# Performance work log

Measured on AMD Instinct MI355X. Metric: run time of the kernel, lower is better.

## Reference

```python
import jax, jax.numpy as jnp
import numpy as np

EMB = 1024
NUM_HEADS = 16


def setup_inputs() -> dict:
    key = jax.random.key(0)
    k_x, k_k, k_q, k_v, k_u, k_b = jax.random.split(key, 6)
    b, s, e = 4, 2048, EMB
    lim = 1.0 / np.sqrt(e)
    return {
        "x": jax.random.normal(k_x, (b, s, e), dtype=jnp.float32),
        "Wk": jax.random.uniform(k_k, (e, e), jnp.float32, -lim, lim),
        "Wq": jax.random.uniform(k_q, (e, e), jnp.float32, -lim, lim),
        "Wv": jax.random.uniform(k_v, (e, e), jnp.float32, -lim, lim),
        "Wu": jax.random.uniform(k_u, (e, e), jnp.float32, -lim, lim),
        "bu": jax.random.uniform(k_b, (e,), jnp.float32, -lim, lim),
    }


def reference(x, Wk, Wq, Wv, Wu, bu):
    b, s, e = x.shape
    h = NUM_HEADS
    d = e // h
    # scale q and k each by emb**(-1/4), as in the original (note: emb, not head_size)
    scale = e ** -0.25
    # project and split heads: (b, h, s, d)
    q = (x @ Wq.T).reshape(b, s, h, d).transpose(0, 2, 1, 3) * scale
    k = (x @ Wk.T).reshape(b, s, h, d).transpose(0, 2, 1, 3) * scale
    v = (x @ Wv.T).reshape(b, s, h, d).transpose(0, 2, 1, 3)
    # attention scores (b, h, s, s)
    dot = jnp.einsum("bhqd,bhkd->bhqk", q, k)
    # causal mask: strictly-upper triangle (offset=1) set to -inf
    causal = jnp.triu(jnp.ones((s, s), dtype=bool), k=1)
    dot = jnp.where(causal[None, None, :, :], -jnp.inf, dot)
    attn = jax.nn.softmax(dot, axis=-1)
    out = jnp.einsum("bhqk,bhkd->bhqd", attn, v)
    out = out.transpose(0, 2, 1, 3).reshape(b, s, e)
    return out @ Wu.T + bu
```

## Files before the change

kernel.cpp:

```cpp
#include <hip/hip_runtime.h>
#include <stdint.h>
#include <math.h>


typedef __attribute__((ext_vector_type(8))) short bf16x8;
typedef __attribute__((ext_vector_type(4))) float f32x4;
typedef __attribute__((ext_vector_type(16))) float f32x16;
typedef __attribute__((ext_vector_type(4))) int i32x4;
typedef __attribute__((ext_vector_type(4))) short s16x4;

#define GLOAD_LDS16(gp, lp)                                                     \
  __builtin_amdgcn_global_load_lds(                                             \
      (__attribute__((address_space(1))) void*)(gp),                            \
      (__attribute__((address_space(3))) void*)(lp), 16, 0, 0)

__device__ __forceinline__ short f2bf(float f) {
  union { float f; uint32_t u; } v; v.f = f;
  uint32_t r = v.u + 0x7FFFu + ((v.u >> 16) & 1u);
  return (short)(r >> 16);
}
__device__ __forceinline__ float bf2f(short s) {
  union { uint32_t u; float f; } v; v.u = ((uint32_t)(uint16_t)s) << 16;
  return v.f;
}
__device__ __forceinline__ short f2bfn(float f) {
  union { __bf16 h; short s; } u; u.h = (__bf16)f; return u.s;
}
__device__ __forceinline__ uint32_t pk2n(float a, float b) {
  union { __bf16 h[2]; uint32_t u; } v;
  v.h[0] = (__bf16)a; v.h[1] = (__bf16)b;
  return v.u;
}

__device__ __forceinline__ void swap32(uint32_t a, uint32_t b, int hi,
                                       uint32_t& out0, uint32_t& out1) {
#if __has_builtin(__builtin_amdgcn_permlane32_swap)
  typedef __attribute__((ext_vector_type(2))) int i32x2;
  i32x2 r = __builtin_amdgcn_permlane32_swap((int)a, (int)b, false, false);
  out0 = (uint32_t)r.x; out1 = (uint32_t)r.y;
#else
  uint32_t ta = (uint32_t)__shfl_xor((int)a, 32);
  uint32_t tb = (uint32_t)__shfl_xor((int)b, 32);
  out0 = hi ? tb : a;
  out1 = hi ? b : ta;
#endif
}

__global__ __launch_bounds__(256) void cast_all_kernel(const float* __restrict__ x,
                                                       const float* __restrict__ w0,
                                                       const float* __restrict__ w1,
                                                       const float* __restrict__ w2,
                                                       const float* __restrict__ w3,
                                                       short* __restrict__ xb,
                                                       short* o0, short* o1, short* o2, short* o3) {
  int bid = blockIdx.x;
  const float* src;
  short* dst;
  int i;
  if (bid < 4096) {
    src = x; dst = xb;
    i = (bid * 256 + threadIdx.x) * 8;
  } else {
    int r = bid - 4096;
    int wsel = r >> 9, blk = r & 511;
    src = (wsel == 0) ? w0 : (wsel == 1) ? w1 : (wsel == 2) ? w2 : w3;
    dst = (wsel == 0) ? o0 : (wsel == 1) ? o1 : (wsel == 2) ? o2 : o3;
    i = (blk * 256 + threadIdx.x) * 8;
  }
  const float4* s = (const float4*)(src + i);
  float4 f0 = s[0], f1 = s[1];
  bf16x8 o;
  o[0] = f2bf(f0.x); o[1] = f2bf(f0.y); o[2] = f2bf(f0.z); o[3] = f2bf(f0.w);
  o[4] = f2bf(f1.x); o[5] = f2bf(f1.y); o[6] = f2bf(f1.z); o[7] = f2bf(f1.w);
  *(bf16x8*)(dst + i) = o;
}

template <int MODE>
__device__ __forceinline__ void gemm_bt_core(short* __restrict__ a_lds,
                                             short* __restrict__ b_lds,
                                             const short* __restrict__ A,
                                             const short* __restrict__ Bm,
                                             short* __restrict__ Cb,
                                             float* __restrict__ Cf,
                                             const float* __restrict__ bias,
                                             int row0, int col0) {
  const float QSCALE = 0.03125f * 1.44269504f;
  const int tid = threadIdx.x;
  const int w = tid >> 6, l = tid & 63;
  const int l15 = l & 15, lhi = l >> 4;
  const int wr = w >> 1, wc = w & 1;

  f32x4 acc[4][4];
#pragma unroll
  for (int m = 0; m < 4; ++m)
#pragma unroll
    for (int n = 0; n < 4; ++n)
      acc[m][n] = (f32x4){0.f, 0.f, 0.f, 0.f};

  const int o0 = tid * 16;
  const int sr = o0 >> 7;
  const int sc = o0 & 127;

  for (int kt = 0; kt < 16; ++kt) {
    const char* Ab = (const char*)A + (size_t)(row0 + sr) * 2048 + kt * 128 + sc;
    const char* Bb = (const char*)Bm + (size_t)(col0 + sr) * 2048 + kt * 128 + sc;
#pragma unroll
    for (int i = 0; i < 4; ++i) {
      GLOAD_LDS16(Ab + (size_t)i * 32 * 2048, (char*)a_lds + i * 4096 + o0);
      GLOAD_LDS16(Bb + (size_t)i * 32 * 2048, (char*)b_lds + i * 4096 + o0);
    }
    __syncthreads();
#pragma unroll
    for (int kk = 0; kk < 2; ++kk) {
      bf16x8 af[4], bg[4];
#pragma unroll
      for (int m = 0; m < 4; ++m) {
        int r = wr * 64 + m * 16 + l15;
        af[m] = *(const bf16x8*)((const char*)a_lds + r * 128 + kk * 64 + lhi * 16);
      }
#pragma unroll
      for (int n = 0; n < 4; ++n) {
        int r = wc * 64 + n * 16 + l15;
        bg[n] = *(const bf16x8*)((const char*)b_lds + r * 128 + kk * 64 + lhi * 16);
      }
#pragma unroll
      for (int m = 0; m < 4; ++m)
#pragma unroll
        for (int n = 0; n < 4; ++n)
          acc[m][n] = __builtin_amdgcn_mfma_f32_16x16x32_bf16(af[m], bg[n], acc[m][n], 0, 0, 0);
    }
    __syncthreads();
  }

  if constexpr (MODE == 3) {
#pragma unroll
    for (int m = 0; m < 4; ++m)
#pragma unroll
      for (int n = 0; n < 4; ++n) {
        int colg = col0 + wc * 64 + n * 16 + l15;
#pragma unroll
        for (int r = 0; r < 4; ++r) {
          int rowg = row0 + wr * 64 + m * 16 + lhi * 4 + r;
          Cf[(size_t)rowg * 1024 + colg] = acc[m][n][r] + bias[colg];
        }
      }
  } else {
    const int bidx = row0 >> 11;
    const int hh = (col0 >> 6) + wc;
    const int t_base = ((row0 & 2047) + wr * 64) >> 5;
    const size_t base = ((size_t)(bidx * 16 + hh) * 64 + t_base) * 2048;
    if constexpr (MODE == 2) {
      const size_t c0 = base + (lhi >> 1) * 256 + l15 * 8 + (lhi & 1) * 4;
#pragma unroll
      for (int m = 0; m < 4; ++m)
#pragma unroll
        for (int n = 0; n < 4; ++n) {
          size_t idx = c0 + (size_t)(m >> 1) * 2048 + ((n >> 1) * 2 + (m & 1)) * 512 + (n & 1) * 128;
          s16x4 vv;
#pragma unroll
          for (int r = 0; r < 4; ++r) vv[r] = f2bfn(acc[m][n][r]);
          *(s16x4*)(Cb + idx) = vv;
        }
    } else {
      const size_t c0 = base + (l15 >> 3) * 256 + lhi * 32 + (l15 & 7);
#pragma unroll
      for (int m = 0; m < 4; ++m)
#pragma unroll
        for (int n = 0; n < 4; ++n) {
          size_t idx = c0 + (size_t)(m >> 1) * 2048 + n * 512 + (m & 1) * 128;
#pragma unroll
          for (int r = 0; r < 4; ++r)
            Cb[idx + r * 8] = f2bfn(MODE == 0 ? acc[m][n][r] * QSCALE : acc[m][n][r]);
        }
    }
  }
}

__global__ __launch_bounds__(256) void gemm_qkv_kernel(const short* __restrict__ xb,
                                                       const short* __restrict__ wq,
                                                       const short* __restrict__ wk,
                                                       const short* __restrict__ wv,
                                                       short* qf, short* kf, short* vf) {
  __shared__ short a_lds[128 * 64];
  __shared__ short b_lds[128 * 64];
  int f = blockIdx.x;
  int g = f & 7, j = f >> 3;
  int rowb = g * 8 + (j & 7);
  int cz = j >> 3;
  int colb = cz & 7, z = cz >> 3;
  int row0 = rowb * 128, col0 = colb * 128;
  if (z == 0)      gemm_bt_core<0>(a_lds, b_lds, xb, wq, qf, nullptr, nullptr, row0, col0);
  else if (z == 1) gemm_bt_core<1>(a_lds, b_lds, xb, wk, kf, nullptr, nullptr, row0, col0);
  else             gemm_bt_core<2>(a_lds, b_lds, xb, wv, vf, nullptr, nullptr, row0, col0);
}

__global__ __launch_bounds__(256) void gemm_out_kernel(const short* __restrict__ ob,
                                                       const short* __restrict__ wu,
                                                       const float* __restrict__ bias,
                                                       float* __restrict__ out) {
  __shared__ short a_lds[128 * 64];
  __shared__ short b_lds[128 * 64];
  int f = blockIdx.x;
  int g = f & 7, j = f >> 3;
  int row0 = (g * 8 + (j & 7)) * 128;
  int col0 = (j >> 3) * 128;
  gemm_bt_core<3>(a_lds, b_lds, ob, wu, nullptr, out, bias, row0, col0);
}

__global__ __launch_bounds__(512) void attn_kernel(const short* __restrict__ qf,
                                                   const short* __restrict__ kf,
                                                   const short* __restrict__ vf,
                                                   short* __restrict__ ob) {
  int bh = blockIdx.x;
  int b = bh >> 4, h = bh & 15;
  int tid = threadIdx.x;
  int wid = tid >> 6, l = tid & 63;
  int l31 = l & 31, hi = l >> 5;
  int pair = blockIdx.y * 4 + (wid >> 1);
  int team = wid & 1;
  int slot = wid >> 1;

  __shared__ float mrg[4][64][34];

  const short* qfb = qf + (size_t)bh * 131072;
  const short* kfb = kf + (size_t)bh * 131072;
  const short* vfb = vf + (size_t)bh * 131072;

  for (int part = 0; part < 2; ++part) {
    int sidx = part ? (63 - pair) : pair;
    int qrow0 = sidx * 32;
    int qg = qrow0 + l31;
    int n = sidx + 1;
    int t0 = team ? (n >> 1) : 0;
    int t1 = team ? n : (n >> 1);

    bf16x8 aq[4];
    {
      const short* qp = qfb + sidx * 2048 + l * 8;
#pragma unroll
      for (int s = 0; s < 4; ++s) aq[s] = *(const bf16x8*)(qp + s * 512);
    }

    f32x16 o_lo = {}, o_hi = {};
    float lsum = 0.f;

    if (t0 < t1) {
      const short* kp = kfb + (size_t)t0 * 2048 + l * 8;
      const short* vp = vfb + (size_t)t0 * 2048 + l * 8;
      bf16x8 kc[4];
#pragma unroll
      for (int s = 0; s < 4; ++s) kc[s] = *(const bf16x8*)(kp + s * 512);

      for (int t = t0; t < t1; ++t) {
        bf16x8 vc[4];
#pragma unroll
        for (int s = 0; s < 4; ++s) vc[s] = *(const bf16x8*)(vp + s * 512);
        vp += 2048;

        f32x16 st = {};
        __builtin_amdgcn_s_setprio(1);
#pragma unroll
        for (int s = 0; s < 4; ++s)
          st = __builtin_amdgcn_mfma_f32_32x32x16_bf16(kc[s], aq[s], st, 0, 0, 0);
        __builtin_amdgcn_s_setprio(0);

        kp += 2048;
        {
          const short* kpc = (t + 1 < t1) ? kp : (kp - 2048);
#pragma unroll
          for (int s = 0; s < 4; ++s) kc[s] = *(const bf16x8*)(kpc + s * 512);
        }

        if (t == sidx) {
#pragma unroll
          for (int r = 0; r < 16; ++r) {
            int kk = qrow0 + (r & 3) + 8 * (r >> 2) + 4 * hi;
            if (kk > qg) st[r] = -INFINITY;
          }
        }

#pragma unroll
        for (int r = 0; r < 16; ++r) st[r] = exp2f(st[r]);

        float sm[8];
#pragma unroll
        for (int r = 0; r < 8; ++r) sm[r] = st[r] + st[r + 8];
#pragma unroll
        for (int r = 0; r < 4; ++r) sm[r] += sm[r + 4];
        lsum += (sm[0] + sm[1]) + (sm[2] + sm[3]);

        uint32_t a0, a2, b1, b3, c0, c2, d1, d3;
        swap32(pk2n(st[0], st[1]),   pk2n(st[4], st[5]),   hi, a0, a2);
        swap32(pk2n(st[2], st[3]),   pk2n(st[6], st[7]),   hi, b1, b3);
        swap32(pk2n(st[8], st[9]),   pk2n(st[12], st[13]), hi, c0, c2);
        swap32(pk2n(st[10], st[11]), pk2n(st[14], st[15]), hi, d1, d3);
        i32x4 u0 = {(int)a0, (int)b1, (int)a2, (int)b3};
        i32x4 u1 = {(int)c0, (int)d1, (int)c2, (int)d3};
        bf16x8 pa0 = __builtin_bit_cast(bf16x8, u0);
        bf16x8 pa1 = __builtin_bit_cast(bf16x8, u1);

        __builtin_amdgcn_s_setprio(1);
        o_lo = __builtin_amdgcn_mfma_f32_32x32x16_bf16(vc[0], pa0, o_lo, 0, 0, 0);
        o_lo = __builtin_amdgcn_mfma_f32_32x32x16_bf16(vc[1], pa1, o_lo, 0, 0, 0);
        o_hi = __builtin_amdgcn_mfma_f32_32x32x16_bf16(vc[2], pa0, o_hi, 0, 0, 0);
        o_hi = __builtin_amdgcn_mfma_f32_32x32x16_bf16(vc[3], pa1, o_hi, 0, 0, 0);
        __builtin_amdgcn_s_setprio(0);
      }
    }

    lsum += __shfl_xor(lsum, 32);

    if (team == 1) {
      float* pp = &mrg[slot][l][0];
#pragma unroll
      for (int r = 0; r < 16; ++r) { pp[r] = o_lo[r]; pp[16 + r] = o_hi[r]; }
      pp[32] = lsum;
    }
    __syncthreads();
    if (team == 0) {
      const float* pp = &mrg[slot][l][0];
      float inv = 1.0f / (lsum + pp[32]);
      short* obase = ob + (size_t)(b * 2048 + qg) * 1024 + h * 64;
#pragma unroll
      for (int g = 0; g < 4; ++g) {
        int d0 = 8 * g + 4 * hi;
        s16x4 v0, v1;
#pragma unroll
        for (int jj = 0; jj < 4; ++jj) {
          v0[jj] = f2bfn((o_lo[4 * g + jj] + pp[4 * g + jj]) * inv);
          v1[jj] = f2bfn((o_hi[4 * g + jj] + pp[16 + 4 * g + jj]) * inv);
        }
        *(s16x4*)(obase + d0) = v0;
        *(s16x4*)(obase + 32 + d0) = v1;
      }
    }
    __syncthreads();
  }
}

extern "C" void kernel_launch(void* const* d_in, const int* in_sizes, int n_in,
                              void* d_out, int out_size, void* d_ws, size_t ws_size,
                              hipStream_t stream) {
  const float* x  = (const float*)d_in[0];
  const float* Wk = (const float*)d_in[1];
  const float* Wq = (const float*)d_in[2];
  const float* Wv = (const float*)d_in[3];
  const float* Wu = (const float*)d_in[4];
  const float* bu = (const float*)d_in[5];
  float* out = (float*)d_out;

  char* ws = (char*)d_ws;
  const size_t MB = 1u << 20;
  short* xb  = (short*)(ws + 0 * MB);
  short* qf  = (short*)(ws + 16 * MB);
  short* kfb = (short*)(ws + 32 * MB);
  short* vfb = (short*)(ws + 48 * MB);
  short* ob  = (short*)(ws + 64 * MB);
  short* wqb = (short*)(ws + 80 * MB);
  short* wkb = (short*)(ws + 82 * MB);
  short* wvb = (short*)(ws + 84 * MB);
  short* wub = (short*)(ws + 86 * MB);

  cast_all_kernel<<<6144, 256, 0, stream>>>(x, Wq, Wk, Wv, Wu, xb, wqb, wkb, wvb, wub);
  gemm_qkv_kernel<<<1536, 256, 0, stream>>>(xb, wqb, wkb, wvb, qf, kfb, vfb);
  attn_kernel<<<dim3(64, 8), 512, 0, stream>>>(qf, kfb, vfb, ob);
  gemm_out_kernel<<<512, 256, 0, stream>>>(ob, wub, bu, out);
}
```

Baseline: 175.4 us.

## Triple-buffer GEMM K-loop with async LDS prefetch two tiles ahead

Restructures the shared GEMM core from a synchronous 64-wide K tile (load, sync, compute, sync) into a 32-wide K tile with three LDS buffers. Global-to-LDS loads run two iterations ahead, and a single vmcnt wait plus barrier per step replaces the two __syncthreads. The aim is to hide global memory latency behind MFMA work in both the QKV and output projection GEMMs. In exchange there are more, smaller iterations, slightly more LDS (48KB vs 32KB), and reliance on manual waitcnt counting.

```diff
diff --git a/kernel.cpp b/kernel.cpp
--- a/kernel.cpp
+++ b/kernel.cpp
@@ -97,40 +97,55 @@
     for (int n = 0; n < 4; ++n)
       acc[m][n] = (f32x4){0.f, 0.f, 0.f, 0.f};
 
-  const int o0 = tid * 16;
-  const int sr = o0 >> 7;
-  const int sc = o0 & 127;
-
-  for (int kt = 0; kt < 16; ++kt) {
-    const char* Ab = (const char*)A + (size_t)(row0 + sr) * 2048 + kt * 128 + sc;
-    const char* Bb = (const char*)Bm + (size_t)(col0 + sr) * 2048 + kt * 128 + sc;
-#pragma unroll
-    for (int i = 0; i < 4; ++i) {
-      GLOAD_LDS16(Ab + (size_t)i * 32 * 2048, (char*)a_lds + i * 4096 + o0);
-      GLOAD_LDS16(Bb + (size_t)i * 32 * 2048, (char*)b_lds + i * 4096 + o0);
-    }
-    __syncthreads();
-#pragma unroll
-    for (int kk = 0; kk < 2; ++kk) {
-      bf16x8 af[4], bg[4];
-#pragma unroll
-      for (int m = 0; m < 4; ++m) {
-        int r = wr * 64 + m * 16 + l15;
-        af[m] = *(const bf16x8*)((const char*)a_lds + r * 128 + kk * 64 + lhi * 16);
-      }
-#pragma unroll
-      for (int n = 0; n < 4; ++n) {
-        int r = wc * 64 + n * 16 + l15;
-        bg[n] = *(const bf16x8*)((const char*)b_lds + r * 128 + kk * 64 + lhi * 16);
-      }
-#pragma unroll
-      for (int m = 0; m < 4; ++m)
-#pragma unroll
-        for (int n = 0; n < 4; ++n)
-          acc[m][n] = __builtin_amdgcn_mfma_f32_16x16x32_bf16(af[m], bg[n], acc[m][n], 0, 0, 0);
-    }
-    __syncthreads();
+  const int o2 = tid * 16;
+  const int r0 = o2 >> 6;
+  const int cbyte = o2 & 63;
+  const char* Ab0 = (const char*)A + (size_t)(row0 + r0) * 2048 + cbyte;
+  const char* Ab1 = Ab0 + (size_t)64 * 2048;
+  const char* Bb0 = (const char*)Bm + (size_t)(col0 + r0) * 2048 + cbyte;
+  const char* Bb1 = Bb0 + (size_t)64 * 2048;
+
+#define GSTG(t, buf) do {                                                     \
+    GLOAD_LDS16(Ab0 + (size_t)(t) * 64, (char*)a_lds + (buf) * 8192 + o2);    \
+    GLOAD_LDS16(Ab1 + (size_t)(t) * 64, (char*)a_lds + (buf) * 8192 + 4096 + o2); \
+    GLOAD_LDS16(Bb0 + (size_t)(t) * 64, (char*)b_lds + (buf) * 8192 + o2);    \
+    GLOAD_LDS16(Bb1 + (size_t)(t) * 64, (char*)b_lds + (buf) * 8192 + 4096 + o2); \
+  } while (0)
+
+  GSTG(0, 0);
+  GSTG(1, 1);
+  asm volatile("s_waitcnt vmcnt(4)" ::: "memory");
+  __builtin_amdgcn_s_barrier();
+  __builtin_amdgcn_sched_barrier(0);
+
+  int c = 0, cs = 2;
+  for (int kt = 0; kt < 32; ++kt) {
+    if (kt + 2 < 32) GSTG(kt + 2, cs);
+    const char* ab = (const char*)a_lds + c * 8192;
+    const char* bb = (const char*)b_lds + c * 8192;
+    bf16x8 af[4], bg[4];
+#pragma unroll
+    for (int m = 0; m < 4; ++m)
+      af[m] = *(const bf16x8*)(ab + (wr * 64 + m * 16 + l15) * 64 + lhi * 16);
+#pragma unroll
+    for (int n = 0; n < 4; ++n)
+      bg[n] = *(const bf16x8*)(bb + (wc * 64 + n * 16 + l15) * 64 + lhi * 16);
+#pragma unroll
+    for (int m = 0; m < 4; ++m)
+#pragma unroll
+      for (int n = 0; n < 4; ++n)
+        acc[m][n] = __builtin_amdgcn_mfma_f32_16x16x32_bf16(af[m], bg[n], acc[m][n], 0, 0, 0);
+    if (kt + 2 < 32) {
+      asm volatile("s_waitcnt vmcnt(4)" ::: "memory");
+    } else {
+      asm volatile("s_waitcnt vmcnt(0)" ::: "memory");
+    }
+    __builtin_amdgcn_s_barrier();
+    __builtin_amdgcn_sched_barrier(0);
+    c = (c == 2) ? 0 : c + 1;
+    cs = (cs == 2) ? 0 : cs + 1;
   }
+#undef GSTG
 
   if constexpr (MODE == 3) {
 #pragma unroll
@@ -181,8 +196,8 @@
                                                        const short* __restrict__ wk,
                                                        const short* __restrict__ wv,
                                                        short* qf, short* kf, short* vf) {
-  __shared__ short a_lds[128 * 64];
-  __shared__ short b_lds[128 * 64];
+  __shared__ short a_lds[3 * 4096];
+  __shared__ short b_lds[3 * 4096];
   int f = blockIdx.x;
   int g = f & 7, j = f >> 3;
   int rowb = g * 8 + (j & 7);
@@ -198,8 +213,8 @@
                                                        const short* __restrict__ wu,
                                                        const float* __restrict__ bias,
                                                        float* __restrict__ out) {
-  __shared__ short a_lds[128 * 64];
-  __shared__ short b_lds[128 * 64];
+  __shared__ short a_lds[3 * 4096];
+  __shared__ short b_lds[3 * 4096];
   int f = blockIdx.x;
   int g = f & 7, j = f >> 3;
   int row0 = (g * 8 + (j & 7)) * 128;
```

New measurement: 177.4 us. About the same (+1.1%).
